# Performance work log

Measured on AMD Instinct MI355X. Metric: run time of the kernel, lower is better.

Reference implementation:

```python
import jax, jax.numpy as jnp
import numpy as np

N = 50000      # nodes
E = 400000     # edges (before self loops)
F_IN = 128     # num_features
HID = 64       # hidden_dim
HEADS = 4
G = 64         # number of graphs in batch
NCLS = 2
NEG = 0.2      # leaky relu negative slope
BN_EPS = 1e-5


def setup_inputs() -> dict:
    key = jax.random.key(0)
    ks = jax.random.split(key, 32)
    rn = lambda k, shape, s=0.05: jax.random.normal(k, shape, jnp.float32) * s
    inp = {}
    inp["x"] = jax.random.normal(ks[0], (N, F_IN), jnp.float32)
    inp["edge_index"] = jax.random.randint(ks[1], (2, E), 0, N, dtype=jnp.int32)
    inp["batch"] = jnp.sort(jax.random.randint(ks[2], (N,), 0, G, dtype=jnp.int32))
    # layer 0 GATConv (concat=True) + pre projection
    inp["conv0_W"] = rn(ks[3], (F_IN, HEADS * HID))
    inp["conv0_att_src"] = rn(ks[4], (HEADS, HID))
    inp["conv0_att_dst"] = rn(ks[5], (HEADS, HID))
    inp["conv0_bias"] = jnp.zeros((HEADS * HID,), jnp.float32)
    inp["pre0_W"] = rn(ks[6], (HEADS * HID, HID))
    inp["pre0_b"] = jnp.zeros((HID,), jnp.float32)
    # layers 1..2 GATConv (concat=False), stacked
    inp["convs_W"] = rn(ks[7], (2, HID, HEADS * HID))
    inp["convs_att_src"] = rn(ks[8], (2, HEADS, HID))
    inp["convs_att_dst"] = rn(ks[9], (2, HEADS, HID))
    inp["convs_bias"] = jnp.zeros((2, HID), jnp.float32)
    # batch norms (eval mode: running stats)
    inp["bn_gamma"] = jnp.ones((3, HID), jnp.float32)
    inp["bn_beta"] = jnp.zeros((3, HID), jnp.float32)
    inp["bn_mean"] = rn(ks[10], (3, HID), 0.1)
    inp["bn_var"] = jax.random.uniform(ks[11], (3, HID), jnp.float32) + 0.5
    # JK projection, attention pooling, classifier
    inp["jump_W"] = rn(ks[12], (3 * HID, HID))
    inp["jump_b"] = jnp.zeros((HID,), jnp.float32)
    inp["att_W"] = rn(ks[13], (HID, 1))
    inp["att_b"] = jnp.zeros((1,), jnp.float32)
    inp["cls_W1"] = rn(ks[14], (HID, HID // 2))
    inp["cls_b1"] = jnp.zeros((HID // 2,), jnp.float32)
    inp["cls_W2"] = rn(ks[15], (HID // 2, NCLS))
    inp["cls_b2"] = jnp.zeros((NCLS,), jnp.float32)
    return inp


def _segment_softmax(logits, seg, num_segments):
    m = jax.ops.segment_max(logits, seg, num_segments=num_segments)
    e = jnp.exp(logits - m[seg])
    s = jax.ops.segment_sum(e, seg, num_segments=num_segments)
    return e / s[seg]


def _gat_conv(x, src, dst, W, a_src, a_dst, bias, concat):
    n = x.shape[0]
    H, C = a_src.shape
    xh = (x @ W).reshape(n, H, C)                         # [N, H, C]
    as_n = jnp.einsum('nhc,hc->nh', xh, a_src)            # [N, H]
    ad_n = jnp.einsum('nhc,hc->nh', xh, a_dst)            # [N, H]
    logits = jax.nn.leaky_relu(as_n[src] + ad_n[dst], NEG)  # [E', H]
    att = _segment_softmax(logits, dst, n)                # softmax over incoming edges
    out = jax.ops.segment_sum(xh[src] * att[:, :, None], dst, num_segments=n)
    out = out.reshape(n, H * C) if concat else out.mean(axis=1)
    return out + bias


def _bn(h, g, b, m, v):
    return (h - m) * jax.lax.rsqrt(v + BN_EPS) * g + b


def reference(x, edge_index, batch, conv0_W, conv0_att_src, conv0_att_dst,
              conv0_bias, pre0_W, pre0_b, convs_W, convs_att_src, convs_att_dst,
              convs_bias, bn_gamma, bn_beta, bn_mean, bn_var, jump_W, jump_b,
              att_W, att_b, cls_W1, cls_b1, cls_W2, cls_b2):
    n = x.shape[0]
    loops = jnp.arange(n, dtype=edge_index.dtype)
    src = jnp.concatenate([edge_index[0], loops])         # add_self_loops=True
    dst = jnp.concatenate([edge_index[1], loops])
    reps = []
    # layer 0: concat heads -> pre projection -> BN -> ELU (no residual: 128 != 64)
    h = _gat_conv(x, src, dst, conv0_W, conv0_att_src, conv0_att_dst, conv0_bias, True)
    h = h @ pre0_W + pre0_b
    h = jax.nn.elu(_bn(h, bn_gamma[0], bn_beta[0], bn_mean[0], bn_var[0]))
    reps.append(h)
    # layers 1..2: mean heads -> BN -> ELU -> residual
    for i in range(2):
        h_in = h
        h = _gat_conv(h, src, dst, convs_W[i], convs_att_src[i], convs_att_dst[i],
                      convs_bias[i], False)
        h = jax.nn.elu(_bn(h, bn_gamma[i + 1], bn_beta[i + 1], bn_mean[i + 1], bn_var[i + 1]))
        h = h + h_in
        reps.append(h)
    # jumping knowledge (cat)
    h = jnp.concatenate(reps, axis=-1) @ jump_W + jump_b  # [N, HID]
    # attentional global pooling
    a = _segment_softmax((h @ att_W + att_b)[:, 0], batch, G)  # [N]
    hg = jax.ops.segment_sum(h * a[:, None], batch, num_segments=G)  # [G, HID]
    # classifier
    return jax.nn.relu(hg @ cls_W1 + cls_b1) @ cls_W2 + cls_b2
```

## Files before the change

kernel.cpp:

```cpp
#include <hip/hip_runtime.h>
#include <hip/hip_bf16.h>
#include <math.h>

#define NEG 0.2f
#define BNEPS 1e-5f
#define NGRAPH 64
#define SCAN_CHUNK 2048

typedef short bf16x8 __attribute__((ext_vector_type(8)));
typedef float f32x4  __attribute__((ext_vector_type(4)));
typedef float f32x2  __attribute__((ext_vector_type(2)));

__device__ __forceinline__ float bf2f(unsigned short u) {
    return __uint_as_float(((unsigned)u) << 16);
}
__device__ __forceinline__ short f2bf(float f) {
    return (short)__bfloat16_as_ushort(__float2bfloat16(f));
}
__device__ __forceinline__ unsigned char f2fp8(float f) {
    int pk = __builtin_amdgcn_cvt_pk_fp8_f32(f, f, 0, false);
    return (unsigned char)(pk & 0xFF);
}

__global__ __launch_bounds__(256)
void init_kernel(const int* __restrict__ batch, int N,
                 int* __restrict__ counts, int* __restrict__ gstart,
                 float* __restrict__ hg_acc, float* __restrict__ wsum_acc,
                 const float* __restrict__ convs_W,
                 const float* __restrict__ convs_as, const float* __restrict__ convs_ad,
                 float* __restrict__ uv)
{
    int idx = blockIdx.x * 256 + threadIdx.x;
    for (int i = idx; i < N; i += gridDim.x * 256) counts[i] = 0;
    if (blockIdx.x == 0) {
        int t = threadIdx.x;
        for (int i = t; i < NGRAPH * 64; i += 256) hg_acc[i] = 0.f;
        if (t < NGRAPH) wsum_acc[t] = 0.f;
        if (t <= NGRAPH) {
            int lo = 0, hi = N;
            while (lo < hi) {
                int mid = (lo + hi) >> 1;
                if (batch[mid] < t) lo = mid + 1; else hi = mid;
            }
            gstart[t] = lo;
        }
    }
    if (blockIdx.x == 1) {
        int t = threadIdx.x;
        int h = t >> 6, k = t & 63;
        for (int i = 0; i < 2; ++i) {
            const float* Wr  = convs_W + (size_t)i * 64 * 256 + k * 256 + h * 64;
            const float* av  = convs_as + i * 256 + h * 64;
            const float* dv  = convs_ad + i * 256 + h * 64;
            float su = 0.f, sv = 0.f;
            for (int c = 0; c < 64; ++c) { su += Wr[c] * av[c]; sv += Wr[c] * dv[c]; }
            uv[i * 256 + h * 64 + k]       = su;
            uv[512 + i * 256 + h * 64 + k] = sv;
        }
    }
}

__global__ __launch_bounds__(256)
void gemm_xh_mfma(const float* __restrict__ A, int lda,
                  const float* __restrict__ W, int Nc, int M, int K,
                  const float* __restrict__ att_s, const float* __restrict__ att_d,
                  float* __restrict__ as_out, float* __restrict__ ad_out,
                  unsigned char* __restrict__ C8)
{
    __shared__ short Wt[64 * 136];
    const int KP = K + 8;
    int tid  = threadIdx.x;
    int lane = tid & 63, wave = tid >> 6;
    int row0 = blockIdx.x * 64;
    int colb = blockIdx.y * 64;
    int c15 = lane & 15, q = lane >> 4;

    {
        int n = tid & 63;
        for (int k = tid >> 6; k < K; k += 4)
            Wt[n * KP + k] = f2bf(W[(size_t)k * Nc + colb + n]);
    }
    __syncthreads();

    int row = row0 + wave * 16 + c15;
    bool rok = row < M;
    const float* arow = A + (size_t)row * lda + q * 8;

    f32x4 acc[4];
    #pragma unroll
    for (int st = 0; st < 4; ++st) acc[st] = (f32x4){0.f, 0.f, 0.f, 0.f};

    for (int k0 = 0; k0 < K; k0 += 32) {
        bf16x8 av;
        if (rok) {
            float4 a0 = *(const float4*)(arow + k0);
            float4 a1 = *(const float4*)(arow + k0 + 4);
            av[0] = f2bf(a0.x); av[1] = f2bf(a0.y); av[2] = f2bf(a0.z); av[3] = f2bf(a0.w);
            av[4] = f2bf(a1.x); av[5] = f2bf(a1.y); av[6] = f2bf(a1.z); av[7] = f2bf(a1.w);
        } else {
            av = (bf16x8){0,0,0,0,0,0,0,0};
        }
        #pragma unroll
        for (int st = 0; st < 4; ++st) {
            bf16x8 bv = *(const bf16x8*)(Wt + (st * 16 + c15) * KP + k0 + q * 8);
            acc[st] = __builtin_amdgcn_mfma_f32_16x16x32_bf16(av, bv, acc[st], 0, 0, 0);
        }
    }

    #pragma unroll
    for (int r = 0; r < 4; ++r) {
        int orow = row0 + wave * 16 + q * 4 + r;
        if (orow >= M) continue;
        unsigned char* cb = C8 + (size_t)orow * 256 + colb + c15;
        #pragma unroll
        for (int st = 0; st < 4; ++st)
            cb[st * 16] = f2fp8(acc[st][r]);
    }
    float sa[4], da[4];
    #pragma unroll
    for (int st = 0; st < 4; ++st) {
        sa[st] = att_s[colb + st * 16 + c15];
        da[st] = att_d[colb + st * 16 + c15];
    }
    #pragma unroll
    for (int r = 0; r < 4; ++r) {
        float ps = acc[0][r] * sa[0] + acc[1][r] * sa[1] + acc[2][r] * sa[2] + acc[3][r] * sa[3];
        float pd = acc[0][r] * da[0] + acc[1][r] * da[1] + acc[2][r] * da[2] + acc[3][r] * da[3];
        #pragma unroll
        for (int o = 1; o < 16; o <<= 1) {
            ps += __shfl_xor(ps, o);
            pd += __shfl_xor(pd, o);
        }
        int orow = row0 + wave * 16 + q * 4 + r;
        if (c15 == 0 && orow < M) {
            as_out[orow * 4 + blockIdx.y] = ps;
            ad_out[orow * 4 + blockIdx.y] = pd;
        }
    }
}

__global__ __launch_bounds__(256)
void gemm_n64_mfma(const void* __restrict__ Araw, int lda, int a_is_bf16,
                   const float* __restrict__ W, int w_gat, int M, int K,
                   const float* __restrict__ bias, float scale,
                   float* __restrict__ C, int ldc, int mode,
                   const float* __restrict__ bn_g, const float* __restrict__ bn_b,
                   const float* __restrict__ bn_m, const float* __restrict__ bn_v,
                   const float* __restrict__ resid, int ldr,
                   unsigned char* __restrict__ h8_out,
                   const float* __restrict__ u, const float* __restrict__ v,
                   float* __restrict__ as_out, float* __restrict__ ad_out,
                   const float* __restrict__ attW, const float* __restrict__ attb,
                   const int* __restrict__ batch,
                   float* __restrict__ hg_acc, float* __restrict__ wsum_acc)
{
    __shared__ short Wt[64 * 264];
    const int KP = K + 8;
    int tid  = threadIdx.x;
    int lane = tid & 63, wave = tid >> 6;
    int row0 = blockIdx.x * 64;
    int c15 = lane & 15, q = lane >> 4;

    {
        int n = tid & 63;
        for (int k = tid >> 6; k < K; k += 4) {
            int widx = w_gat ? ((k & 63) * 256 + (k >> 6) * 64 + n) : (k * 64 + n);
            Wt[n * KP + k] = f2bf(W[widx]);
        }
    }
    __syncthreads();

    int row = row0 + wave * 16 + c15;
    bool rok = row < M;

    f32x4 acc[4];
    #pragma unroll
    for (int st = 0; st < 4; ++st) acc[st] = (f32x4){0.f, 0.f, 0.f, 0.f};

    for (int k0 = 0; k0 < K; k0 += 32) {
        bf16x8 av;
        if (rok) {
            if (a_is_bf16) {
                av = *(const bf16x8*)((const unsigned short*)Araw
                                      + (size_t)row * lda + k0 + q * 8);
            } else {
                const float* ap = (const float*)Araw + (size_t)row * lda + k0 + q * 8;
                float4 a0 = *(const float4*)ap;
                float4 a1 = *(const float4*)(ap + 4);
                av[0] = f2bf(a0.x); av[1] = f2bf(a0.y); av[2] = f2bf(a0.z); av[3] = f2bf(a0.w);
                av[4] = f2bf(a1.x); av[5] = f2bf(a1.y); av[6] = f2bf(a1.z); av[7] = f2bf(a1.w);
            }
        } else {
            av = (bf16x8){0,0,0,0,0,0,0,0};
        }
        #pragma unroll
        for (int st = 0; st < 4; ++st) {
            bf16x8 bv = *(const bf16x8*)(Wt + (st * 16 + c15) * KP + k0 + q * 8);
            acc[st] = __builtin_amdgcn_mfma_f32_16x16x32_bf16(av, bv, acc[st], 0, 0, 0);
        }
    }

    #pragma unroll
    for (int st = 0; st < 4; ++st) {
        int col = st * 16 + c15;
        float bs = bias ? bias[col] : 0.f;
        float sg = 1.f, sb = 0.f;
        if (mode == 1) {
            sg = bn_g[col] / sqrtf(bn_v[col] + BNEPS);
            sb = bn_b[col] - bn_m[col] * sg;
        }
        #pragma unroll
        for (int r = 0; r < 4; ++r) {
            int orow = row0 + wave * 16 + q * 4 + r;
            if (orow >= M) continue;
            float vvv = acc[st][r] * scale + bs;
            if (mode == 1) {
                vvv = vvv * sg + sb;
                vvv = vvv > 0.f ? vvv : __expf(vvv) - 1.f;
            }
            if (resid) vvv += resid[(size_t)orow * ldr + col];
            acc[st][r] = vvv;
            if (C) C[(size_t)orow * ldc + col] = vvv;
        }
    }

    if (h8_out) {
        #pragma unroll
        for (int r = 0; r < 4; ++r) {
            int orow = row0 + wave * 16 + q * 4 + r;
            if (orow >= M) continue;
            unsigned char* hb = h8_out + (size_t)orow * 64 + c15;
            #pragma unroll
            for (int st = 0; st < 4; ++st)
                hb[st * 16] = f2fp8(acc[st][r]);
        }
    }

    if (u) {
        float uu[4][4], vv2[4][4];
        #pragma unroll
        for (int h = 0; h < 4; ++h)
            #pragma unroll
            for (int st = 0; st < 4; ++st) {
                uu[h][st]  = u[h * 64 + st * 16 + c15];
                vv2[h][st] = v[h * 64 + st * 16 + c15];
            }
        #pragma unroll
        for (int r = 0; r < 4; ++r) {
            int orow = row0 + wave * 16 + q * 4 + r;
            float pv[8];
            #pragma unroll
            for (int h = 0; h < 4; ++h) {
                pv[h]     = acc[0][r] * uu[h][0] + acc[1][r] * uu[h][1]
                          + acc[2][r] * uu[h][2] + acc[3][r] * uu[h][3];
                pv[4 + h] = acc[0][r] * vv2[h][0] + acc[1][r] * vv2[h][1]
                          + acc[2][r] * vv2[h][2] + acc[3][r] * vv2[h][3];
            }
            #pragma unroll
            for (int j = 0; j < 4; ++j) {
                float send = (c15 & 8) ? pv[j] : pv[j + 4];
                float keep = (c15 & 8) ? pv[j + 4] : pv[j];
                pv[j] = keep + __shfl_xor(send, 8);
            }
            #pragma unroll
            for (int j = 0; j < 2; ++j) {
                float send = (c15 & 4) ? pv[j] : pv[j + 2];
                float keep = (c15 & 4) ? pv[j + 2] : pv[j];
                pv[j] = keep + __shfl_xor(send, 4);
            }
            {
                float send = (c15 & 2) ? pv[0] : pv[1];
                float keep = (c15 & 2) ? pv[1] : pv[0];
                pv[0] = keep + __shfl_xor(send, 2);
            }
            pv[0] += __shfl_xor(pv[0], 1);
            if ((c15 & 1) == 0 && orow < M) {
                int jj = c15 >> 1;
                if (jj < 4) as_out[orow * 4 + jj] = pv[0];
                else        ad_out[orow * 4 + (jj - 4)] = pv[0];
            }
        }
// ... 71 lines not shown
}

__global__ __launch_bounds__(256)
void scan_phase1(const int* __restrict__ counts, int N, int* __restrict__ blocksum)
{
    __shared__ int wsum[4];
    int tid = threadIdx.x, lane = tid & 63, wave = tid >> 6;
    int base = blockIdx.x * SCAN_CHUNK;
    int s = 0;
    #pragma unroll
    for (int j = 0; j < SCAN_CHUNK / 256; ++j) {
        int idx = base + tid + j * 256;
        if (idx < N) s += counts[idx];
    }
    #pragma unroll
    for (int o = 32; o; o >>= 1) s += __shfl_xor(s, o);
    if (lane == 0) wsum[wave] = s;
    __syncthreads();
    if (tid == 0) blocksum[blockIdx.x] = wsum[0] + wsum[1] + wsum[2] + wsum[3];
}

__global__ __launch_bounds__(256)
void scan_phase3(const int* __restrict__ counts, int N, int nb,
                 const int* __restrict__ blocksum,
                 int* __restrict__ rowptr, int* __restrict__ cursor)
{
    __shared__ int wsum[4];
    __shared__ int pref[64];
    int tid = threadIdx.x, lane = tid & 63, wave = tid >> 6;

    if (wave == 0) {
        int v = (lane < nb) ? blocksum[lane] : 0;
        int incl = v;
        #pragma unroll
        for (int o = 1; o < 64; o <<= 1) {
            int t = __shfl_up(incl, o);
            if (lane >= o) incl += t;
        }
        pref[lane] = incl;
    }
    __syncthreads();
    int boff = blockIdx.x ? pref[blockIdx.x - 1] : 0;
    if (blockIdx.x == 0 && tid == 0) rowptr[N] = pref[nb - 1];

    int start = blockIdx.x * SCAN_CHUNK + tid * 8;
    int v[8];
    int s = 0;
    #pragma unroll
    for (int j = 0; j < 8; ++j) {
        v[j] = (start + j < N) ? counts[start + j] : 0;
        s += v[j];
    }
    int incl = s;
    #pragma unroll
    for (int o = 1; o < 64; o <<= 1) {
        int t = __shfl_up(incl, o);
        if (lane >= o) incl += t;
    }
    if (lane == 63) wsum[wave] = incl;
    __syncthreads();
    int woff = 0;
    #pragma unroll
    for (int w = 0; w < 4; ++w) if (w < wave) woff += wsum[w];
    int run = boff + woff + incl - s;
    #pragma unroll
    for (int j = 0; j < 8; ++j) {
        int idx = start + j;
        if (idx < N) { rowptr[idx] = run; cursor[idx] = run; }
        run += v[j];
    }
}

__global__ __launch_bounds__(256)
void scatter_kernel(const int* __restrict__ ei, int E, int N,
                    int* __restrict__ cursor, int* __restrict__ csr_src)
{
    int e = blockIdx.x * blockDim.x + threadIdx.x;
    int Etot = E + N;
    if (e >= Etot) return;
    int s, d;
    if (e < E) { s = ei[e]; d = ei[E + e]; } else { s = d = e - E; }
    int pos = atomicAdd(&cursor[d], 1);
    csr_src[pos] = s;
}

__global__ __launch_bounds__(256)
void aggregate_kernel(const int* __restrict__ rowptr, const int* __restrict__ csr_src,
                      const float* __restrict__ as_n, const float* __restrict__ ad_n,
                      const unsigned char* __restrict__ xh8,
                      const float* __restrict__ bias,
                      unsigned short* __restrict__ outp, int N)
{
    int node = (blockIdx.x * blockDim.x + threadIdx.x) >> 6;
    int lane = threadIdx.x & 63;
    if (node >= N) return;
    int h = lane >> 4, li = lane & 15, grp = lane & 48;
    int e0 = rowptr[node], e1 = rowptr[node + 1];
    float adh = ad_n[node * 4 + h];
    unsigned laneoff = (unsigned)(lane * 4);

    float4 acc = make_float4(0.f, 0.f, 0.f, 0.f);
    float wsum = 0.f;

    for (int base = e0; base < e1; base += 16) {
        int cnt = e1 - base; if (cnt > 16) cnt = 16;
        int s = 0; float w = 0.f;
        if (li < cnt) {
            s = csr_src[base + li];
            float l = as_n[s * 4 + h] + adh;
            l = fmaxf(l, NEG * l);
            w = __expf(l);
        }
        int k = 0;
        for (; k + 3 < cnt; k += 4) {
            float w0 = __shfl(w, grp + k),     w1 = __shfl(w, grp + k + 1);
            float w2 = __shfl(w, grp + k + 2), w3 = __shfl(w, grp + k + 3);
            int s0 = __shfl(s, grp + k),       s1 = __shfl(s, grp + k + 1);
            int s2 = __shfl(s, grp + k + 2),   s3 = __shfl(s, grp + k + 3);
            unsigned x0 = *(const unsigned*)(xh8 + ((unsigned)s0 * 256u + laneoff));
            unsigned x1 = *(const unsigned*)(xh8 + ((unsigned)s1 * 256u + laneoff));
            unsigned x2 = *(const unsigned*)(xh8 + ((unsigned)s2 * 256u + laneoff));
            unsigned x3 = *(const unsigned*)(xh8 + ((unsigned)s3 * 256u + laneoff));
            f32x2 l0 = __builtin_amdgcn_cvt_pk_f32_fp8((int)x0, false);
            f32x2 h0 = __builtin_amdgcn_cvt_pk_f32_fp8((int)x0, true);
            f32x2 l1 = __builtin_amdgcn_cvt_pk_f32_fp8((int)x1, false);
            f32x2 h1 = __builtin_amdgcn_cvt_pk_f32_fp8((int)x1, true);
            f32x2 l2 = __builtin_amdgcn_cvt_pk_f32_fp8((int)x2, false);
            f32x2 h2 = __builtin_amdgcn_cvt_pk_f32_fp8((int)x2, true);
            f32x2 l3 = __builtin_amdgcn_cvt_pk_f32_fp8((int)x3, false);
            f32x2 h3 = __builtin_amdgcn_cvt_pk_f32_fp8((int)x3, true);
            acc.x += w0 * l0.x; acc.y += w0 * l0.y; acc.z += w0 * h0.x; acc.w += w0 * h0.y;
            acc.x += w1 * l1.x; acc.y += w1 * l1.y; acc.z += w1 * h1.x; acc.w += w1 * h1.y;
            acc.x += w2 * l2.x; acc.y += w2 * l2.y; acc.z += w2 * h2.x; acc.w += w2 * h2.y;
            acc.x += w3 * l3.x; acc.y += w3 * l3.y; acc.z += w3 * h3.x; acc.w += w3 * h3.y;
            wsum += (w0 + w1) + (w2 + w3);
        }
        for (; k < cnt; ++k) {
            float wk = __shfl(w, grp + k);
            int sk = __shfl(s, grp + k);
            unsigned xv = *(const unsigned*)(xh8 + ((unsigned)sk * 256u + laneoff));
            f32x2 lo = __builtin_amdgcn_cvt_pk_f32_fp8((int)xv, false);
            f32x2 hi = __builtin_amdgcn_cvt_pk_f32_fp8((int)xv, true);
            acc.x += wk * lo.x; acc.y += wk * lo.y;
            acc.z += wk * hi.x; acc.w += wk * hi.y;
            wsum += wk;
        }
    }

    float rw = 1.f / wsum;
    float4 bs = *(const float4*)(bias + lane * 4);
    ushort4 pk;
    pk.x = (unsigned short)f2bf(acc.x * rw + bs.x);
    pk.y = (unsigned short)f2bf(acc.y * rw + bs.y);
    pk.z = (unsigned short)f2bf(acc.z * rw + bs.z);
    pk.w = (unsigned short)f2bf(acc.w * rw + bs.w);
    *(ushort4*)(outp + (size_t)node * 256 + lane * 4) = pk;
}

__global__ __launch_bounds__(256)
void aggregate_z(const int* __restrict__ rowptr, const int* __restrict__ csr_src,
                 const float* __restrict__ as_n, const float* __restrict__ ad_n,
                 const unsigned char* __restrict__ h8,
                 unsigned short* __restrict__ zout, int N)
{
    int node = (blockIdx.x * blockDim.x + threadIdx.x) >> 6;
    int lane = threadIdx.x & 63;
    if (node >= N) return;
    int h = lane >> 4, li = lane & 15, grp = lane & 48;
    int e0 = rowptr[node], e1 = rowptr[node + 1];
    float adh = ad_n[node * 4 + h];
    unsigned laneoff = (unsigned)(li * 4);

    float4 acc = make_float4(0.f, 0.f, 0.f, 0.f);
    float wsum = 0.f;

    for (int base = e0; base < e1; base += 16) {
        int cnt = e1 - base; if (cnt > 16) cnt = 16;
        int s = 0; float w = 0.f;
        if (li < cnt) {
            s = csr_src[base + li];
            float l = as_n[s * 4 + h] + adh;
            l = fmaxf(l, NEG * l);
            w = __expf(l);
        }
        int k = 0;
        for (; k + 3 < cnt; k += 4) {
            float w0 = __shfl(w, grp + k),     w1 = __shfl(w, grp + k + 1);
            float w2 = __shfl(w, grp + k + 2), w3 = __shfl(w, grp + k + 3);
            int s0 = __shfl(s, grp + k),       s1 = __shfl(s, grp + k + 1);
            int s2 = __shfl(s, grp + k + 2),   s3 = __shfl(s, grp + k + 3);
            unsigned x0 = *(const unsigned*)(h8 + ((unsigned)s0 * 64u + laneoff));
            unsigned x1 = *(const unsigned*)(h8 + ((unsigned)s1 * 64u + laneoff));
            unsigned x2 = *(const unsigned*)(h8 + ((unsigned)s2 * 64u + laneoff));
            unsigned x3 = *(const unsigned*)(h8 + ((unsigned)s3 * 64u + laneoff));
            f32x2 l0 = __builtin_amdgcn_cvt_pk_f32_fp8((int)x0, false);
            f32x2 h0 = __builtin_amdgcn_cvt_pk_f32_fp8((int)x0, true);
            f32x2 l1 = __builtin_amdgcn_cvt_pk_f32_fp8((int)x1, false);
            f32x2 h1 = __builtin_amdgcn_cvt_pk_f32_fp8((int)x1, true);
            f32x2 l2 = __builtin_amdgcn_cvt_pk_f32_fp8((int)x2, false);
            f32x2 h2 = __builtin_amdgcn_cvt_pk_f32_fp8((int)x2, true);
            f32x2 l3 = __builtin_amdgcn_cvt_pk_f32_fp8((int)x3, false);
            f32x2 h3 = __builtin_amdgcn_cvt_pk_f32_fp8((int)x3, true);
            acc.x += w0 * l0.x; acc.y += w0 * l0.y; acc.z += w0 * h0.x; acc.w += w0 * h0.y;
            acc.x += w1 * l1.x; acc.y += w1 * l1.y; acc.z += w1 * h1.x; acc.w += w1 * h1.y;
            acc.x += w2 * l2.x; acc.y += w2 * l2.y; acc.z += w2 * h2.x; acc.w += w2 * h2.y;
            acc.x += w3 * l3.x; acc.y += w3 * l3.y; acc.z += w3 * h3.x; acc.w += w3 * h3.y;
            wsum += (w0 + w1) + (w2 + w3);
        }
        for (; k < cnt; ++k) {
            float wk = __shfl(w, grp + k);
            int sk = __shfl(s, grp + k);
            unsigned xv = *(const unsigned*)(h8 + ((unsigned)sk * 64u + laneoff));
            f32x2 lo = __builtin_amdgcn_cvt_pk_f32_fp8((int)xv, false);
            f32x2 hi = __builtin_amdgcn_cvt_pk_f32_fp8((int)xv, true);
            acc.x += wk * lo.x; acc.y += wk * lo.y;
            acc.z += wk * hi.x; acc.w += wk * hi.y;
            wsum += wk;
        }
    }

    float rw = 1.f / wsum;
    ushort4 pk;
    pk.x = (unsigned short)f2bf(acc.x * rw);
    pk.y = (unsigned short)f2bf(acc.y * rw);
    pk.z = (unsigned short)f2bf(acc.z * rw);
    pk.w = (unsigned short)f2bf(acc.w * rw);
    *(ushort4*)(zout + (size_t)node * 256 + h * 64 + li * 4) = pk;
}

__global__ void cls_kernel(const float* __restrict__ hg_acc,
                           const float* __restrict__ wsum_acc,
                           const float* __restrict__ W1, const float* __restrict__ b1,
                           const float* __restrict__ W2, const float* __restrict__ b2,
                           float* __restrict__ out)
{
    int g = blockIdx.x, t = threadIdx.x;
    __shared__ float z[32];
    __shared__ float h[64];
    float wsum = wsum_acc[g];
    float rw = (wsum > 0.f) ? 1.f / wsum : 0.f;
    h[t] = hg_acc[g * 64 + t] * rw;
    h[t + 32] = hg_acc[g * 64 + t + 32] * rw;
    __syncthreads();
    float acc = b1[t];
    for (int k = 0; k < 64; ++k) acc += h[k] * W1[k * 32 + t];
    z[t] = fmaxf(acc, 0.f);
    __syncthreads();
    if (t < 2) {
        float o = b2[t];
        for (int j = 0; j < 32; ++j) o += z[j] * W2[j * 2 + t];
        out[g * 2 + t] = o;
    }
}

extern "C" void kernel_launch(void* const* d_in, const int* in_sizes, int n_in,
                              void* d_out, int out_size, void* d_ws, size_t ws_size,
                              hipStream_t stream)
{
    const float* x        = (const float*)d_in[0];
    const int*   ei       = (const int*)d_in[1];
    const int*   batch    = (const int*)d_in[2];
    const float* conv0_W  = (const float*)d_in[3];
    const float* conv0_as = (const float*)d_in[4];
    const float* conv0_ad = (const float*)d_in[5];
    const float* conv0_b  = (const float*)d_in[6];
    const float* pre0_W   = (const float*)d_in[7];
    const float* pre0_b   = (const float*)d_in[8];
    const float* convs_W  = (const float*)d_in[9];
    const float* convs_as = (const float*)d_in[10];
    const float* convs_ad = (const float*)d_in[11];
    const float* convs_b  = (const float*)d_in[12];
    const float* bn_g     = (const float*)d_in[13];
    const float* bn_b     = (const float*)d_in[14];
    const float* bn_m     = (const float*)d_in[15];
    const float* bn_v     = (const float*)d_in[16];
    const float* jump_W   = (const float*)d_in[17];
    const float* jump_b   = (const float*)d_in[18];
    const float* att_W    = (const float*)d_in[19];
    const float* att_b    = (const float*)d_in[20];
    const float* cls_W1   = (const float*)d_in[21];
    const float* cls_b1   = (const float*)d_in[22];
    const float* cls_W2   = (const float*)d_in[23];
    const float* cls_b2   = (const float*)d_in[24];
    float* out = (float*)d_out;

    const int N = in_sizes[0] / 128;
    const int E = in_sizes[1] / 2;
    const int Etot = E + N;
    const int nb = (N + SCAN_CHUNK - 1) / SCAN_CHUNK;

    float* ws      = (float*)d_ws;
    unsigned char* xh8      = (unsigned char*)ws;
    unsigned short* h256_bf = (unsigned short*)ws + (size_t)N * 256;
    float* repsAll = (float*)(h256_bf + (size_t)N * 256);
    float* as_n    = repsAll + (size_t)N * 192;
    float* ad_n    = as_n + (size_t)N * 4;
    float* hg_acc  = ad_n + (size_t)N * 4;
    float* wsum_acc= hg_acc + NGRAPH * 64;
    int*   rowptr  = (int*)(wsum_acc + NGRAPH);
    int*   cursor  = rowptr + (N + 1);
    int*   counts  = cursor + N;
    int*   csr_src = counts + N;
    int*   gstart  = csr_src + Etot;
    int*   blocksum = gstart + (NGRAPH + 1);
    float* uv      = (float*)(blocksum + 64);
    float* as2     = uv + 1024;
    float* ad2     = as2 + (size_t)N * 4;
    unsigned char* h8b = (unsigned char*)(ad2 + (size_t)N * 4);
    unsigned char* h8a = xh8;

    dim3 blk(256);
    int node_wave_blocks = (N + 3) / 4;
    int edge_blocks      = (Etot + 255) / 256;
    int row_blocks       = (N + 63) / 64;

    init_kernel<<<64, blk, 0, stream>>>(batch, N, counts, gstart, hg_acc, wsum_acc,
                                        convs_W, convs_as, convs_ad, uv);
    hist_kernel<<<edge_blocks, blk, 0, stream>>>(ei, E, N, counts);
    scan_phase1<<<nb, blk, 0, stream>>>(counts, N, blocksum);
    scan_phase3<<<nb, blk, 0, stream>>>(counts, N, nb, blocksum, rowptr, cursor);
    scatter_kernel<<<edge_blocks, blk, 0, stream>>>(ei, E, N, cursor, csr_src);

    {
        dim3 g1(row_blocks, 4);
        gemm_xh_mfma<<<g1, blk, 0, stream>>>(x, 128, conv0_W, 256, N, 128,
                                             conv0_as, conv0_ad, as_n, ad_n, xh8);
        aggregate_kernel<<<node_wave_blocks, blk, 0, stream>>>(
            rowptr, csr_src, as_n, ad_n, xh8, conv0_b, h256_bf, N);
        gemm_n64_mfma<<<row_blocks, blk, 0, stream>>>(
            h256_bf, 256, 1, pre0_W, 0, N, 256, pre0_b, 1.f,
            repsAll, 192, 1, bn_g, bn_b, bn_m, bn_v,
            nullptr, 0, h8a, uv, uv + 512, as_n, ad_n,
            nullptr, nullptr, nullptr, nullptr, nullptr);
    }

    aggregate_z<<<node_wave_blocks, blk, 0, stream>>>(rowptr, csr_src, as_n, ad_n,
                                                      h8a, h256_bf, N);
    gemm_n64_mfma<<<row_blocks, blk, 0, stream>>>(
        h256_bf, 256, 1, convs_W, 1, N, 256, convs_b, 0.25f,
        repsAll + 64, 192, 1, bn_g + 64, bn_b + 64, bn_m + 64, bn_v + 64,
        repsAll, 192, h8b, uv + 256, uv + 512 + 256, as2, ad2,
        nullptr, nullptr, nullptr, nullptr, nullptr);

    aggregate_z<<<node_wave_blocks, blk, 0, stream>>>(rowptr, csr_src, as2, ad2,
                                                      h8b, h256_bf, N);
    gemm_n64_mfma<<<row_blocks, blk, 0, stream>>>(
        h256_bf, 256, 1, convs_W + (size_t)64 * 256, 1, N, 256, convs_b + 64, 0.25f,
        repsAll + 128, 192, 1, bn_g + 128, bn_b + 128, bn_m + 128, bn_v + 128,
        repsAll + 64, 192, nullptr, nullptr, nullptr, nullptr, nullptr,
        nullptr, nullptr, nullptr, nullptr, nullptr);

    gemm_n64_mfma<<<row_blocks, blk, 0, stream>>>(
        repsAll, 192, 0, jump_W, 0, N, 192, jump_b, 1.f,
        nullptr, 64, 0, nullptr, nullptr, nullptr, nullptr,
        nullptr, 0, nullptr, nullptr, nullptr, nullptr, nullptr,
        att_W, att_b, batch, hg_acc, wsum_acc);

    cls_kernel<<<NGRAPH, 32, 0, stream>>>(hg_acc, wsum_acc, cls_W1, cls_b1,
                                          cls_W2, cls_b2, out);
}
```

Baseline: 354.5 us.

## Reassociate layer-0 GAT: aggregate raw features, fold conv0_W into pre-projection

```diff
diff --git a/kernel.cpp b/kernel.cpp
--- a/kernel.cpp
+++ b/kernel.cpp
@@ -24,11 +24,17 @@
 
 __global__ __launch_bounds__(256)
 void init_kernel(const int* __restrict__ batch, int N,
-                 int* __restrict__ counts, int* __restrict__ gstart,
+                 int* __restrict__ counts,
                  float* __restrict__ hg_acc, float* __restrict__ wsum_acc,
                  const float* __restrict__ convs_W,
                  const float* __restrict__ convs_as, const float* __restrict__ convs_ad,
-                 float* __restrict__ uv)
+                 const float* __restrict__ conv0_W,
+                 const float* __restrict__ conv0_as, const float* __restrict__ conv0_ad,
+                 const float* __restrict__ conv0_b,
+                 const float* __restrict__ pre0_W, const float* __restrict__ pre0_b,
+                 float* __restrict__ uv,
+                 float* __restrict__ u0, float* __restrict__ v0,
+                 float* __restrict__ Wcomb, float* __restrict__ bias_comb)
 {
     int idx = blockIdx.x * 256 + threadIdx.x;
     for (int i = idx; i < N; i += gridDim.x * 256) counts[i] = 0;
@@ -36,14 +42,6 @@
         int t = threadIdx.x;
         for (int i = t; i < NGRAPH * 64; i += 256) hg_acc[i] = 0.f;
         if (t < NGRAPH) wsum_acc[t] = 0.f;
-        if (t <= NGRAPH) {
-            int lo = 0, hi = N;
-            while (lo < hi) {
-                int mid = (lo + hi) >> 1;
-                if (batch[mid] < t) lo = mid + 1; else hi = mid;
-            }
-            gstart[t] = lo;
-        }
     }
     if (blockIdx.x == 1) {
         int t = threadIdx.x;
@@ -57,86 +55,136 @@
             uv[i * 256 + h * 64 + k]       = su;
             uv[512 + i * 256 + h * 64 + k] = sv;
         }
-    }
-}
-
-__global__ __launch_bounds__(256)
-void gemm_xh_mfma(const float* __restrict__ A, int lda,
-                  const float* __restrict__ W, int Nc, int M, int K,
-                  const float* __restrict__ att_s, const float* __restrict__ att_d,
-                  float* __restrict__ as_out, float* __restrict__ ad_out,
-                  unsigned char* __restrict__ C8)
-{
-    __shared__ short Wt[64 * 136];
-    const int KP = K + 8;
-    int tid  = threadIdx.x;
-    int lane = tid & 63, wave = tid >> 6;
-    int row0 = blockIdx.x * 64;
-    int colb = blockIdx.y * 64;
-    int c15 = lane & 15, q = lane >> 4;
-
-    {
-        int n = tid & 63;
-        for (int k = tid >> 6; k < K; k += 4)
-            Wt[n * KP + k] = f2bf(W[(size_t)k * Nc + colb + n]);
-    }
-    __syncthreads();
-
-    int row = row0 + wave * 16 + c15;
-    bool rok = row < M;
-    const float* arow = A + (size_t)row * lda + q * 8;
-
-    f32x4 acc[4];
-    #pragma unroll
-    for (int st = 0; st < 4; ++st) acc[st] = (f32x4){0.f, 0.f, 0.f, 0.f};
-
-    for (int k0 = 0; k0 < K; k0 += 32) {
-        bf16x8 av;
-        if (rok) {
-            float4 a0 = *(const float4*)(arow + k0);
-            float4 a1 = *(const float4*)(arow + k0 + 4);
-            av[0] = f2bf(a0.x); av[1] = f2bf(a0.y); av[2] = f2bf(a0.z); av[3] = f2bf(a0.w);
-            av[4] = f2bf(a1.x); av[5] = f2bf(a1.y); av[6] = f2bf(a1.z); av[7] = f2bf(a1.w);
-        } else {
-            av = (bf16x8){0,0,0,0,0,0,0,0};
-        }
-        #pragma unroll
-        for (int st = 0; st < 4; ++st) {
-            bf16x8 bv = *(const bf16x8*)(Wt + (st * 16 + c15) * KP + k0 + q * 8);
-            acc[st] = __builtin_amdgcn_mfma_f32_16x16x32_bf16(av, bv, acc[st], 0, 0, 0);
-        }
-    }
-
-    #pragma unroll
-    for (int r = 0; r < 4; ++r) {
-        int orow = row0 + wave * 16 + q * 4 + r;
-        if (orow >= M) continue;
-        unsigned char* cb = C8 + (size_t)orow * 256 + colb + c15;
-        #pragma unroll
-        for (int st = 0; st < 4; ++st)
-            cb[st * 16] = f2fp8(acc[st][r]);
-    }
-    float sa[4], da[4];
-    #pragma unroll
-    for (int st = 0; st < 4; ++st) {
-        sa[st] = att_s[colb + st * 16 + c15];
-        da[st] = att_d[colb + st * 16 + c15];
-    }
-    #pragma unroll
-    for (int r = 0; r < 4; ++r) {
-        float ps = acc[0][r] * sa[0] + acc[1][r] * sa[1] + acc[2][r] * sa[2] + acc[3][r] * sa[3];
-        float pd = acc[0][r] * da[0] + acc[1][r] * da[1] + acc[2][r] * da[2] + acc[3][r] * da[3];
-        #pragma unroll
-        for (int o = 1; o < 16; o <<= 1) {
-            ps += __shfl_xor(ps, o);
-            pd += __shfl_xor(pd, o);
-        }
-        int orow = row0 + wave * 16 + q * 4 + r;
-        if (c15 == 0 && orow < M) {
-            as_out[orow * 4 + blockIdx.y] = ps;
-            ad_out[orow * 4 + blockIdx.y] = pd;
-        }
-    }
+        if (t < 64) {
+            float s = pre0_b[t];
+            for (int c = 0; c < 256; ++c) s += conv0_b[c] * pre0_W[c * 64 + t];
+            bias_comb[t] = s;
+        }
+    }
+    if (blockIdx.x == 2) {
+        int t = threadIdx.x;
+        for (int e = t; e < 512; e += 256) {
+            int h = e >> 7, k = e & 127;
+            const float* Wr = conv0_W + (size_t)k * 256 + h * 64;
+            const float* av = conv0_as + h * 64;
+            const float* dv = conv0_ad + h * 64;
+            float su = 0.f, sv = 0.f;
+            for (int c = 0; c < 64; ++c) { su += Wr[c] * av[c]; sv += Wr[c] * dv[c]; }
+            u0[e] = su; v0[e] = sv;
+        }
+    }
+    if (blockIdx.x >= 3 && blockIdx.x < 11) {
+        int base = (blockIdx.x - 3) * 4096 + threadIdx.x * 16;
+        for (int i = 0; i < 16; ++i) {
+            int e = base + i;
+            int hk = e >> 6, cp = e & 63;
+            int h = hk >> 7, k = hk & 127;
+            const float* Wr = conv0_W + (size_t)k * 256 + h * 64;
+            const float* Pr = pre0_W + (size_t)h * 64 * 64 + cp;
+            float s = 0.f;
+            for (int c = 0; c < 64; ++c) s += Wr[c] * Pr[c * 64];
+            Wcomb[(size_t)hk * 64 + cp] = s;
+        }
+    }
+}
+
+__global__ __launch_bounds__(256)
+void cast_x_kernel(const float* __restrict__ x,
+                   const float* __restrict__ u0, const float* __restrict__ v0,
+                   unsigned char* __restrict__ x8,
+                   float* __restrict__ as_out, float* __restrict__ ad_out, int N)
+{
+    int node = (blockIdx.x * blockDim.x + threadIdx.x) >> 6;
+    int lane = threadIdx.x & 63;
+    if (node >= N) return;
+    float2 xv = *(const float2*)(x + (size_t)node * 128 + lane * 2);
+    int pk = __builtin_amdgcn_cvt_pk_fp8_f32(xv.x, xv.y, 0, false);
+    *(unsigned short*)(x8 + (size_t)node * 128 + lane * 2) = (unsigned short)(pk & 0xFFFF);
+    float p[8];
+    #pragma unroll
+    for (int h = 0; h < 4; ++h) {
+        p[h]     = xv.x * u0[h * 128 + lane * 2] + xv.y * u0[h * 128 + lane * 2 + 1];
+        p[4 + h] = xv.x * v0[h * 128 + lane * 2] + xv.y * v0[h * 128 + lane * 2 + 1];
+    }
+    #pragma unroll
+    for (int j = 0; j < 8; ++j)
+        #pragma unroll
+        for (int o = 1; o < 64; o <<= 1) p[j] += __shfl_xor(p[j], o);
+    if (lane == 0) {
+        #pragma unroll
+        for (int h = 0; h < 4; ++h) {
+            as_out[node * 4 + h] = p[h];
+            ad_out[node * 4 + h] = p[4 + h];
+        }
+    }
+}
+
+__global__ __launch_bounds__(256)
+void aggregate_z0(const int* __restrict__ rowptr, const int* __restrict__ csr_src,
+                  const float* __restrict__ as_n, const float* __restrict__ ad_n,
+                  const unsigned char* __restrict__ x8,
+                  unsigned short* __restrict__ zout, int N)
+{
+    int node = (blockIdx.x * blockDim.x + threadIdx.x) >> 6;
+    int lane = threadIdx.x & 63;
+    if (node >= N) return;
+    int h = lane >> 4, li = lane & 15, grp = lane & 48;
+    int e0 = rowptr[node], e1 = rowptr[node + 1];
+    float adh = ad_n[node * 4 + h];
+    unsigned laneoff = (unsigned)(li * 8);
+
+    float acc[8];
+    #pragma unroll
+    for (int j = 0; j < 8; ++j) acc[j] = 0.f;
+    float wsum = 0.f;
+
+#define ACC_EDGE(wk, xa) {                                                \
+        f32x2 l0 = __builtin_amdgcn_cvt_pk_f32_fp8((int)(xa).x, false);   \
+        f32x2 h0 = __builtin_amdgcn_cvt_pk_f32_fp8((int)(xa).x, true);    \
+        f32x2 l1 = __builtin_amdgcn_cvt_pk_f32_fp8((int)(xa).y, false);   \
+        f32x2 h1 = __builtin_amdgcn_cvt_pk_f32_fp8((int)(xa).y, true);    \
+        acc[0] += (wk) * l0.x; acc[1] += (wk) * l0.y;                     \
+        acc[2] += (wk) * h0.x; acc[3] += (wk) * h0.y;                     \
+        acc[4] += (wk) * l1.x; acc[5] += (wk) * l1.y;                     \
+        acc[6] += (wk) * h1.x; acc[7] += (wk) * h1.y; }
+
+    for (int base = e0; base < e1; base += 16) {
+        int cnt = e1 - base; if (cnt > 16) cnt = 16;
+        int s = 0; float w = 0.f;
+        if (li < cnt) {
+            s = csr_src[base + li];
+            float l = as_n[s * 4 + h] + adh;
+            l = fmaxf(l, NEG * l);
+            w = __expf(l);
+        }
+        int k = 0;
+        for (; k + 3 < cnt; k += 4) {
+            float w0 = __shfl(w, grp + k),     w1 = __shfl(w, grp + k + 1);
+            float w2 = __shfl(w, grp + k + 2), w3 = __shfl(w, grp + k + 3);
+            int s0 = __shfl(s, grp + k),       s1 = __shfl(s, grp + k + 1);
+            int s2 = __shfl(s, grp + k + 2),   s3 = __shfl(s, grp + k + 3);
+            uint2 a0 = *(const uint2*)(x8 + ((size_t)(unsigned)s0 * 128u + laneoff));
+            uint2 a1 = *(const uint2*)(x8 + ((size_t)(unsigned)s1 * 128u + laneoff));
+            uint2 a2 = *(const uint2*)(x8 + ((size_t)(unsigned)s2 * 128u + laneoff));
+            uint2 a3 = *(const uint2*)(x8 + ((size_t)(unsigned)s3 * 128u + laneoff));
+            ACC_EDGE(w0, a0); ACC_EDGE(w1, a1); ACC_EDGE(w2, a2); ACC_EDGE(w3, a3);
+            wsum += (w0 + w1) + (w2 + w3);
+        }
+        for (; k < cnt; ++k) {
+            float wk = __shfl(w, grp + k);
+            int sk = __shfl(s, grp + k);
+            uint2 av = *(const uint2*)(x8 + ((size_t)(unsigned)sk * 128u + laneoff));
+            ACC_EDGE(wk, av);
+            wsum += wk;
+        }
+    }
+#undef ACC_EDGE
+
+    float rw = 1.f / wsum;
+    bf16x8 pk;
+    #pragma unroll
+    for (int j = 0; j < 8; ++j) pk[j] = f2bf(acc[j] * rw);
+    *(bf16x8*)(zout + (size_t)node * 512 + h * 128 + li * 8) = pk;
 }
 
 __global__ __launch_bounds__(256)
@@ -155,21 +203,11 @@
                    float* __restrict__ hg_acc, float* __restrict__ wsum_acc)
 {
     __shared__ short Wt[64 * 264];
-    const int KP = K + 8;
     int tid  = threadIdx.x;
     int lane = tid & 63, wave = tid >> 6;
     int row0 = blockIdx.x * 64;
     int c15 = lane & 15, q = lane >> 4;
 
-    {
-        int n = tid & 63;
-        for (int k = tid >> 6; k < K; k += 4) {
-            int widx = w_gat ? ((k & 63) * 256 + (k >> 6) * 64 + n) : (k * 64 + n);
-            Wt[n * KP + k] = f2bf(W[widx]);
-        }
-    }
-    __syncthreads();
-
     int row = row0 + wave * 16 + c15;
     bool rok = row < M;
 
@@ -177,26 +215,41 @@
     #pragma unroll
     for (int st = 0; st < 4; ++st) acc[st] = (f32x4){0.f, 0.f, 0.f, 0.f};
 
-    for (int k0 = 0; k0 < K; k0 += 32) {
-        bf16x8 av;
-        if (rok) {
-            if (a_is_bf16) {
-                av = *(const bf16x8*)((const unsigned short*)Araw
-                                      + (size_t)row * lda + k0 + q * 8);
+    for (int kc = 0; kc < K; kc += 256) {
+        int CK = K - kc; if (CK > 256) CK = 256;
+        const int KP = CK + 8;
+        __syncthreads();
+        {
+            int n = tid & 63;
+            for (int k = tid >> 6; k < CK; k += 4) {
+                int kk = kc + k;
+                int widx = w_gat ? ((kk & 63) * 256 + (kk >> 6) * 64 + n) : (kk * 64 + n);
+                Wt[n * KP + k] = f2bf(W[widx]);
+            }
+        }
+        __syncthreads();
+
+        for (int k0 = 0; k0 < CK; k0 += 32) {
+            bf16x8 av;
+            if (rok) {
+                if (a_is_bf16) {
+                    av = *(const bf16x8*)((const unsigned short*)Araw
+                                          + (size_t)row * lda + kc + k0 + q * 8);
+                } else {
+                    const float* ap = (const float*)Araw + (size_t)row * lda + kc + k0 + q * 8;
+                    float4 a0 = *(const float4*)ap;
+                    float4 a1 = *(const float4*)(ap + 4);
+                    av[0] = f2bf(a0.x); av[1] = f2bf(a0.y); av[2] = f2bf(a0.z); av[3] = f2bf(a0.w);
+                    av[4] = f2bf(a1.x); av[5] = f2bf(a1.y); av[6] = f2bf(a1.z); av[7] = f2bf(a1.w);
+                }
             } else {
-                const float* ap = (const float*)Araw + (size_t)row * lda + k0 + q * 8;
-                float4 a0 = *(const float4*)ap;
-                float4 a1 = *(const float4*)(ap + 4);
-                av[0] = f2bf(a0.x); av[1] = f2bf(a0.y); av[2] = f2bf(a0.z); av[3] = f2bf(a0.w);
-                av[4] = f2bf(a1.x); av[5] = f2bf(a1.y); av[6] = f2bf(a1.z); av[7] = f2bf(a1.w);
-            }
-        } else {
-            av = (bf16x8){0,0,0,0,0,0,0,0};
-        }
-        #pragma unroll
-        for (int st = 0; st < 4; ++st) {
-            bf16x8 bv = *(const bf16x8*)(Wt + (st * 16 + c15) * KP + k0 + q * 8);
-            acc[st] = __builtin_amdgcn_mfma_f32_16x16x32_bf16(av, bv, acc[st], 0, 0, 0);
+                av = (bf16x8){0,0,0,0,0,0,0,0};
+            }
+            #pragma unroll
+            for (int st = 0; st < 4; ++st) {
+                bf16x8 bv = *(const bf16x8*)(Wt + (st * 16 + c15) * KP + k0 + q * 8);
+                acc[st] = __builtin_amdgcn_mfma_f32_16x16x32_bf16(av, bv, acc[st], 0, 0, 0);
+            }
         }
     }
 
@@ -434,79 +487,6 @@
     if (e < E) { s = ei[e]; d = ei[E + e]; } else { s = d = e - E; }
     int pos = atomicAdd(&cursor[d], 1);
     csr_src[pos] = s;
-}
-
-__global__ __launch_bounds__(256)
-void aggregate_kernel(const int* __restrict__ rowptr, const int* __restrict__ csr_src,
-                      const float* __restrict__ as_n, const float* __restrict__ ad_n,
-                      const unsigned char* __restrict__ xh8,
-                      const float* __restrict__ bias,
-                      unsigned short* __restrict__ outp, int N)
-{
-    int node = (blockIdx.x * blockDim.x + threadIdx.x) >> 6;
-    int lane = threadIdx.x & 63;
-    if (node >= N) return;
-    int h = lane >> 4, li = lane & 15, grp = lane & 48;
-    int e0 = rowptr[node], e1 = rowptr[node + 1];
-    float adh = ad_n[node * 4 + h];
-    unsigned laneoff = (unsigned)(lane * 4);
-
-    float4 acc = make_float4(0.f, 0.f, 0.f, 0.f);
-    float wsum = 0.f;
-
-    for (int base = e0; base < e1; base += 16) {
-        int cnt = e1 - base; if (cnt > 16) cnt = 16;
-        int s = 0; float w = 0.f;
-        if (li < cnt) {
-            s = csr_src[base + li];
-            float l = as_n[s * 4 + h] + adh;
-            l = fmaxf(l, NEG * l);
-            w = __expf(l);
-        }
-        int k = 0;
-        for (; k + 3 < cnt; k += 4) {
-            float w0 = __shfl(w, grp + k),     w1 = __shfl(w, grp + k + 1);
-            float w2 = __shfl(w, grp + k + 2), w3 = __shfl(w, grp + k + 3);
-            int s0 = __shfl(s, grp + k),       s1 = __shfl(s, grp + k + 1);
-            int s2 = __shfl(s, grp + k + 2),   s3 = __shfl(s, grp + k + 3);
-            unsigned x0 = *(const unsigned*)(xh8 + ((unsigned)s0 * 256u + laneoff));
-            unsigned x1 = *(const unsigned*)(xh8 + ((unsigned)s1 * 256u + laneoff));
-            unsigned x2 = *(const unsigned*)(xh8 + ((unsigned)s2 * 256u + laneoff));
-            unsigned x3 = *(const unsigned*)(xh8 + ((unsigned)s3 * 256u + laneoff));
-            f32x2 l0 = __builtin_amdgcn_cvt_pk_f32_fp8((int)x0, false);
-            f32x2 h0 = __builtin_amdgcn_cvt_pk_f32_fp8((int)x0, true);
-            f32x2 l1 = __builtin_amdgcn_cvt_pk_f32_fp8((int)x1, false);
-            f32x2 h1 = __builtin_amdgcn_cvt_pk_f32_fp8((int)x1, true);
-            f32x2 l2 = __builtin_amdgcn_cvt_pk_f32_fp8((int)x2, false);
-            f32x2 h2 = __builtin_amdgcn_cvt_pk_f32_fp8((int)x2, true);
-            f32x2 l3 = __builtin_amdgcn_cvt_pk_f32_fp8((int)x3, false);
-            f32x2 h3 = __builtin_amdgcn_cvt_pk_f32_fp8((int)x3, true);
-            acc.x += w0 * l0.x; acc.y += w0 * l0.y; acc.z += w0 * h0.x; acc.w += w0 * h0.y;
-            acc.x += w1 * l1.x; acc.y += w1 * l1.y; acc.z += w1 * h1.x; acc.w += w1 * h1.y;
-            acc.x += w2 * l2.x; acc.y += w2 * l2.y; acc.z += w2 * h2.x; acc.w += w2 * h2.y;
-            acc.x += w3 * l3.x; acc.y += w3 * l3.y; acc.z += w3 * h3.x; acc.w += w3 * h3.y;
-            wsum += (w0 + w1) + (w2 + w3);
-        }
-        for (; k < cnt; ++k) {
-            float wk = __shfl(w, grp + k);
-            int sk = __shfl(s, grp + k);
-            unsigned xv = *(const unsigned*)(xh8 + ((unsigned)sk * 256u + laneoff));
-            f32x2 lo = __builtin_amdgcn_cvt_pk_f32_fp8((int)xv, false);
-            f32x2 hi = __builtin_amdgcn_cvt_pk_f32_fp8((int)xv, true);
-            acc.x += wk * lo.x; acc.y += wk * lo.y;
-            acc.z += wk * hi.x; acc.w += wk * hi.y;
-            wsum += wk;
-        }
-    }
-
-    float rw = 1.f / wsum;
-    float4 bs = *(const float4*)(bias + lane * 4);
-    ushort4 pk;
-    pk.x = (unsigned short)f2bf(acc.x * rw + bs.x);
-    pk.y = (unsigned short)f2bf(acc.y * rw + bs.y);
-    pk.z = (unsigned short)f2bf(acc.z * rw + bs.z);
-    pk.w = (unsigned short)f2bf(acc.w * rw + bs.w);
-    *(ushort4*)(outp + (size_t)node * 256 + lane * 4) = pk;
 }
 
 __global__ __launch_bounds__(256)
@@ -642,9 +622,8 @@
     const int nb = (N + SCAN_CHUNK - 1) / SCAN_CHUNK;
 
     float* ws      = (float*)d_ws;
-    unsigned char* xh8      = (unsigned char*)ws;
-    unsigned short* h256_bf = (unsigned short*)ws + (size_t)N * 256;
-    float* repsAll = (float*)(h256_bf + (size_t)N * 256);
+    unsigned short* z0 = (unsigned short*)ws;
+    float* repsAll = ws + (size_t)N * 256;
     float* as_n    = repsAll + (size_t)N * 192;
     float* ad_n    = as_n + (size_t)N * 4;
     float* hg_acc  = ad_n + (size_t)N * 4;
@@ -653,51 +632,54 @@
     int*   cursor  = rowptr + (N + 1);
     int*   counts  = cursor + N;
     int*   csr_src = counts + N;
-    int*   gstart  = csr_src + Etot;
-    int*   blocksum = gstart + (NGRAPH + 1);
+    int*   blocksum = csr_src + Etot;
     float* uv      = (float*)(blocksum + 64);
-    float* as2     = uv + 1024;
+    float* u0      = uv + 1024;
+    float* v0      = u0 + 512;
+    float* Wcomb   = v0 + 512;
+    float* bias_comb = Wcomb + 512 * 64;
+    float* as2     = bias_comb + 64;
     float* ad2     = as2 + (size_t)N * 4;
-    unsigned char* h8b = (unsigned char*)(ad2 + (size_t)N * 4);
-    unsigned char* h8a = xh8;
+    unsigned char* x8  = (unsigned char*)(ad2 + (size_t)N * 4);
+    unsigned char* h8a = x8 + (size_t)N * 128;
+    unsigned char* h8b = h8a + (size_t)N * 64;
 
     dim3 blk(256);
     int node_wave_blocks = (N + 3) / 4;
     int edge_blocks      = (Etot + 255) / 256;
     int row_blocks       = (N + 63) / 64;
 
-    init_kernel<<<64, blk, 0, stream>>>(batch, N, counts, gstart, hg_acc, wsum_acc,
-                                        convs_W, convs_as, convs_ad, uv);
+    init_kernel<<<64, blk, 0, stream>>>(batch, N, counts, hg_acc, wsum_acc,
+                                        convs_W, convs_as, convs_ad,
+                                        conv0_W, conv0_as, conv0_ad, conv0_b,
+                                        pre0_W, pre0_b,
+                                        uv, u0, v0, Wcomb, bias_comb);
     hist_kernel<<<edge_blocks, blk, 0, stream>>>(ei, E, N, counts);
     scan_phase1<<<nb, blk, 0, stream>>>(counts, N, blocksum);
     scan_phase3<<<nb, blk, 0, stream>>>(counts, N, nb, blocksum, rowptr, cursor);
     scatter_kernel<<<edge_blocks, blk, 0, stream>>>(ei, E, N, cursor, csr_src);
 
-    {
-        dim3 g1(row_blocks, 4);
-        gemm_xh_mfma<<<g1, blk, 0, stream>>>(x, 128, conv0_W, 256, N, 128,
-                                             conv0_as, conv0_ad, as_n, ad_n, xh8);
-        aggregate_kernel<<<node_wave_blocks, blk, 0, stream>>>(
-            rowptr, csr_src, as_n, ad_n, xh8, conv0_b, h256_bf, N);
-        gemm_n64_mfma<<<row_blocks, blk, 0, stream>>>(
-            h256_bf, 256, 1, pre0_W, 0, N, 256, pre0_b, 1.f,
-            repsAll, 192, 1, bn_g, bn_b, bn_m, bn_v,
-            nullptr, 0, h8a, uv, uv + 512, as_n, ad_n,
-            nullptr, nullptr, nullptr, nullptr, nullptr);
-    }
+    cast_x_kernel<<<node_wave_blocks, blk, 0, stream>>>(x, u0, v0, x8, as_n, ad_n, N);
+    aggregate_z0<<<node_wave_blocks, blk, 0, stream>>>(rowptr, csr_src, as_n, ad_n,
+                                                       x8, z0, N);
+    gemm_n64_mfma<<<row_blocks, blk, 0, stream>>>(
+        z0, 512, 1, Wcomb, 0, N, 512, bias_comb, 1.f,
+        repsAll, 192, 1, bn_g, bn_b, bn_m, bn_v,
+        nullptr, 0, h8a, uv, uv + 512, as_n, ad_n,
+        nullptr, nullptr, nullptr, nullptr, nullptr);
 
     aggregate_z<<<node_wave_blocks, blk, 0, stream>>>(rowptr, csr_src, as_n, ad_n,
-                                                      h8a, h256_bf, N);
+                                                      h8a, z0, N);
     gemm_n64_mfma<<<row_blocks, blk, 0, stream>>>(
-        h256_bf, 256, 1, convs_W, 1, N, 256, convs_b, 0.25f,
+        z0, 256, 1, convs_W, 1, N, 256, convs_b, 0.25f,
         repsAll + 64, 192, 1, bn_g + 64, bn_b + 64, bn_m + 64, bn_v + 64,
         repsAll, 192, h8b, uv + 256, uv + 512 + 256, as2, ad2,
         nullptr, nullptr, nullptr, nullptr, nullptr);
 
     aggregate_z<<<node_wave_blocks, blk, 0, stream>>>(rowptr, csr_src, as2, ad2,
-                                                      h8b, h256_bf, N);
+                                                      h8b, z0, N);
     gemm_n64_mfma<<<row_blocks, blk, 0, stream>>>(
-        h256_bf, 256, 1, convs_W + (size_t)64 * 256, 1, N, 256, convs_b + 64, 0.25f,
+        z0, 256, 1, convs_W + (size_t)64 * 256, 1, N, 256, convs_b + 64, 0.25f,
         repsAll + 128, 192, 1, bn_g + 128, bn_b + 128, bn_m + 128, bn_v + 128,
         repsAll + 64, 192, nullptr, nullptr, nullptr, nullptr, nullptr,
         nullptr, nullptr, nullptr, nullptr, nullptr);
```

New measurement: 402.8 us. +13.6%, slower.

## Loop over column blocks inside xh GEMM to reuse A-row loads; drop gstart

Applied to the files above, without the earlier changes.

```diff
diff --git a/kernel.cpp b/kernel.cpp
--- a/kernel.cpp
+++ b/kernel.cpp
@@ -24,7 +24,7 @@
 
 __global__ __launch_bounds__(256)
 void init_kernel(const int* __restrict__ batch, int N,
-                 int* __restrict__ counts, int* __restrict__ gstart,
+                 int* __restrict__ counts,
                  float* __restrict__ hg_acc, float* __restrict__ wsum_acc,
                  const float* __restrict__ convs_W,
                  const float* __restrict__ convs_as, const float* __restrict__ convs_ad,
@@ -36,14 +36,6 @@
         int t = threadIdx.x;
         for (int i = t; i < NGRAPH * 64; i += 256) hg_acc[i] = 0.f;
         if (t < NGRAPH) wsum_acc[t] = 0.f;
-        if (t <= NGRAPH) {
-            int lo = 0, hi = N;
-            while (lo < hi) {
-                int mid = (lo + hi) >> 1;
-                if (batch[mid] < t) lo = mid + 1; else hi = mid;
-            }
-            gstart[t] = lo;
-        }
     }
     if (blockIdx.x == 1) {
         int t = threadIdx.x;
@@ -72,69 +64,79 @@
     int tid  = threadIdx.x;
     int lane = tid & 63, wave = tid >> 6;
     int row0 = blockIdx.x * 64;
-    int colb = blockIdx.y * 64;
     int c15 = lane & 15, q = lane >> 4;
-
-    {
-        int n = tid & 63;
-        for (int k = tid >> 6; k < K; k += 4)
-            Wt[n * KP + k] = f2bf(W[(size_t)k * Nc + colb + n]);
-    }
-    __syncthreads();
 
     int row = row0 + wave * 16 + c15;
     bool rok = row < M;
     const float* arow = A + (size_t)row * lda + q * 8;
 
-    f32x4 acc[4];
-    #pragma unroll
-    for (int st = 0; st < 4; ++st) acc[st] = (f32x4){0.f, 0.f, 0.f, 0.f};
-
-    for (int k0 = 0; k0 < K; k0 += 32) {
-        bf16x8 av;
+    bf16x8 avk[4];
+    #pragma unroll
+    for (int kk = 0; kk < 4; ++kk) {
         if (rok) {
-            float4 a0 = *(const float4*)(arow + k0);
-            float4 a1 = *(const float4*)(arow + k0 + 4);
-            av[0] = f2bf(a0.x); av[1] = f2bf(a0.y); av[2] = f2bf(a0.z); av[3] = f2bf(a0.w);
-            av[4] = f2bf(a1.x); av[5] = f2bf(a1.y); av[6] = f2bf(a1.z); av[7] = f2bf(a1.w);
+            float4 a0 = *(const float4*)(arow + kk * 32);
+            float4 a1 = *(const float4*)(arow + kk * 32 + 4);
+            avk[kk][0] = f2bf(a0.x); avk[kk][1] = f2bf(a0.y);
+            avk[kk][2] = f2bf(a0.z); avk[kk][3] = f2bf(a0.w);
+            avk[kk][4] = f2bf(a1.x); avk[kk][5] = f2bf(a1.y);
+            avk[kk][6] = f2bf(a1.z); avk[kk][7] = f2bf(a1.w);
         } else {
-            av = (bf16x8){0,0,0,0,0,0,0,0};
-        }
+            avk[kk] = (bf16x8){0,0,0,0,0,0,0,0};
+        }
+    }
+
+    for (int cb = 0; cb < 4; ++cb) {
+        int colb = cb * 64;
+        __syncthreads();
+        {
+            int n = tid & 63;
+            for (int k = tid >> 6; k < K; k += 4)
+                Wt[n * KP + k] = f2bf(W[(size_t)k * Nc + colb + n]);
+        }
+        __syncthreads();
+
+        f32x4 acc[4];
+        #pragma unroll
+        for (int st = 0; st < 4; ++st) acc[st] = (f32x4){0.f, 0.f, 0.f, 0.f};
+
+        #pragma unroll
+        for (int kk = 0; kk < 4; ++kk) {
+            #pragma unroll
+            for (int st = 0; st < 4; ++st) {
+                bf16x8 bv = *(const bf16x8*)(Wt + (st * 16 + c15) * KP + kk * 32 + q * 8);
+                acc[st] = __builtin_amdgcn_mfma_f32_16x16x32_bf16(avk[kk], bv, acc[st], 0, 0, 0);
+            }
+        }
+
+        #pragma unroll
+        for (int r = 0; r < 4; ++r) {
+            int orow = row0 + wave * 16 + q * 4 + r;
+            if (orow >= M) continue;
+            unsigned char* cb8 = C8 + (size_t)orow * 256 + colb + c15;
+            #pragma unroll
+            for (int st = 0; st < 4; ++st)
+                cb8[st * 16] = f2fp8(acc[st][r]);
+        }
+        float sa[4], da[4];
         #pragma unroll
         for (int st = 0; st < 4; ++st) {
-            bf16x8 bv = *(const bf16x8*)(Wt + (st * 16 + c15) * KP + k0 + q * 8);
-            acc[st] = __builtin_amdgcn_mfma_f32_16x16x32_bf16(av, bv, acc[st], 0, 0, 0);
-        }
-    }
-
-    #pragma unroll
-    for (int r = 0; r < 4; ++r) {
-        int orow = row0 + wave * 16 + q * 4 + r;
-        if (orow >= M) continue;
-        unsigned char* cb = C8 + (size_t)orow * 256 + colb + c15;
-        #pragma unroll
-        for (int st = 0; st < 4; ++st)
-            cb[st * 16] = f2fp8(acc[st][r]);
-    }
-    float sa[4], da[4];
-    #pragma unroll
-    for (int st = 0; st < 4; ++st) {
-        sa[st] = att_s[colb + st * 16 + c15];
-        da[st] = att_d[colb + st * 16 + c15];
-    }
-    #pragma unroll
-    for (int r = 0; r < 4; ++r) {
-        float ps = acc[0][r] * sa[0] + acc[1][r] * sa[1] + acc[2][r] * sa[2] + acc[3][r] * sa[3];
-        float pd = acc[0][r] * da[0] + acc[1][r] * da[1] + acc[2][r] * da[2] + acc[3][r] * da[3];
-        #pragma unroll
-        for (int o = 1; o < 16; o <<= 1) {
-            ps += __shfl_xor(ps, o);
-            pd += __shfl_xor(pd, o);
-        }
-        int orow = row0 + wave * 16 + q * 4 + r;
-        if (c15 == 0 && orow < M) {
-            as_out[orow * 4 + blockIdx.y] = ps;
-            ad_out[orow * 4 + blockIdx.y] = pd;
+            sa[st] = att_s[colb + st * 16 + c15];
+            da[st] = att_d[colb + st * 16 + c15];
+        }
+        #pragma unroll
+        for (int r = 0; r < 4; ++r) {
+            float ps = acc[0][r] * sa[0] + acc[1][r] * sa[1] + acc[2][r] * sa[2] + acc[3][r] * sa[3];
+            float pd = acc[0][r] * da[0] + acc[1][r] * da[1] + acc[2][r] * da[2] + acc[3][r] * da[3];
+            #pragma unroll
+            for (int o = 1; o < 16; o <<= 1) {
+                ps += __shfl_xor(ps, o);
+                pd += __shfl_xor(pd, o);
+            }
+            int orow = row0 + wave * 16 + q * 4 + r;
+            if (c15 == 0 && orow < M) {
+                as_out[orow * 4 + cb] = ps;
+                ad_out[orow * 4 + cb] = pd;
+            }
         }
     }
 }
@@ -653,8 +655,7 @@
     int*   cursor  = rowptr + (N + 1);
     int*   counts  = cursor + N;
     int*   csr_src = counts + N;
-    int*   gstart  = csr_src + Etot;
-    int*   blocksum = gstart + (NGRAPH + 1);
+    int*   blocksum = csr_src + Etot;
     float* uv      = (float*)(blocksum + 64);
     float* as2     = uv + 1024;
     float* ad2     = as2 + (size_t)N * 4;
@@ -666,7 +667,7 @@
     int edge_blocks      = (Etot + 255) / 256;
     int row_blocks       = (N + 63) / 64;
 
-    init_kernel<<<64, blk, 0, stream>>>(batch, N, counts, gstart, hg_acc, wsum_acc,
+    init_kernel<<<64, blk, 0, stream>>>(batch, N, counts, hg_acc, wsum_acc,
                                         convs_W, convs_as, convs_ad, uv);
     hist_kernel<<<edge_blocks, blk, 0, stream>>>(ei, E, N, counts);
     scan_phase1<<<nb, blk, 0, stream>>>(counts, N, blocksum);
@@ -674,9 +675,8 @@
     scatter_kernel<<<edge_blocks, blk, 0, stream>>>(ei, E, N, cursor, csr_src);
 
     {
-        dim3 g1(row_blocks, 4);
-        gemm_xh_mfma<<<g1, blk, 0, stream>>>(x, 128, conv0_W, 256, N, 128,
-                                             conv0_as, conv0_ad, as_n, ad_n, xh8);
+        gemm_xh_mfma<<<row_blocks, blk, 0, stream>>>(x, 128, conv0_W, 256, N, 128,
+                                                     conv0_as, conv0_ad, as_n, ad_n, xh8);
         aggregate_kernel<<<node_wave_blocks, blk, 0, stream>>>(
             rowptr, csr_src, as_n, ad_n, xh8, conv0_b, h256_bf, N);
         gemm_n64_mfma<<<row_blocks, blk, 0, stream>>>(
```

After: 358.5 us. About the same (+1.1%).
